# Kernel tuning notes

Hardware: AMD Instinct MI355X
Metric: run time of the kernel (lower is better)

The kernel has to match this reference:

```python
import jax, jax.numpy as jnp
import numpy as np

NUM_CLASSES = 16384
FEATURE_DIM = 128
LAMBDA_PARAM = 0.005
EPS = 1e-12  # matches torch F.normalize clamp_min eps


def setup_inputs() -> dict:
    key = jax.random.key(0)
    k1, k2 = jax.random.split(key)
    z = jax.random.normal(k1, (NUM_CLASSES, FEATURE_DIM), dtype=jnp.float32)
    labels = jax.random.randint(k2, (NUM_CLASSES,), 0, NUM_CLASSES, dtype=jnp.int32)
    return {"z": z, "labels": labels}


def _l2_normalize(x):
    # torch F.normalize(dim=1): x / max(||x||, eps); zero rows stay zero.
    n = jnp.linalg.norm(x, axis=1, keepdims=True)
    return x / jnp.maximum(n, EPS)


def reference(z, labels):
    # per-class mean via single segment reduce (replaces the per-class python loop)
    counts = jax.ops.segment_sum(jnp.ones_like(labels, dtype=z.dtype), labels,
                                 num_segments=NUM_CLASSES)            # [C]
    sums = jax.ops.segment_sum(z, labels, num_segments=NUM_CLASSES)   # [C, D]
    has = counts > 0
    centers = jnp.where(has[:, None], sums / jnp.maximum(counts, 1.0)[:, None], 0.0)

    z_norm = _l2_normalize(z)                 # [B, D]
    centers_norm = _l2_normalize(centers)     # [C, D]
    batch_size = z.shape[0]
    c = (z_norm @ centers_norm.T) / batch_size  # [B, C], square since B == C

    diag = jnp.diagonal(c)
    invariance_loss = jnp.sum((diag - 1.0) ** 2)
    redundancy_reduction_loss = jnp.sum(c ** 2) - jnp.sum(diag ** 2)  # off-diagonal sq sum
    return invariance_loss + LAMBDA_PARAM * redundancy_reduction_loss
```

## Files before the change

### kernel.cpp

```cpp
#include <hip/hip_runtime.h>
#include <hip/hip_fp16.h>

#define NC 16384
#define FD 128
#define LAMBDA 0.005f
#define SLOTCAP 64
#define NCH 256

typedef __attribute__((ext_vector_type(8))) short short8;
typedef __attribute__((ext_vector_type(4))) float f32x4;

__device__ __forceinline__ float wave_sum(float v) {
#pragma unroll
  for (int m = 32; m > 0; m >>= 1) v += __shfl_xor(v, m, 64);
  return v;
}

__global__ __launch_bounds__(256) void zero_kernel(int4* __restrict__ cnt4,
                                                   float* __restrict__ scal) {
  cnt4[blockIdx.x * 256 + threadIdx.x] = make_int4(0, 0, 0, 0);
  if (blockIdx.x == 0 && threadIdx.x < 16) scal[threadIdx.x] = 0.f;
}

__global__ __launch_bounds__(256) void scatter_kernel(
    const int* __restrict__ labels, int* __restrict__ cnt, int* __restrict__ slot) {
  int i = blockIdx.x * 256 + threadIdx.x;
  int lab = labels[i];
  int p = atomicAdd(&cnt[lab], 1);
  if (p < SLOTCAP) slot[(size_t)lab * SLOTCAP + p] = i;
}

__global__ __launch_bounds__(256) void center_kernel(
    const float* __restrict__ z, const int* __restrict__ cnt,
    const int* __restrict__ slot, float* __restrict__ cn,
    float2* __restrict__ dpart) {
  __shared__ float red[8];
  int t = threadIdx.x, wave = t >> 6, lane = t & 63;
  int c = blockIdx.x * 4 + wave;

  int n = cnt[c];
  if (n > SLOTCAP) n = SLOTCAP;
  float2 s = make_float2(0.f, 0.f);
  for (int k = 0; k < n; ++k) {
    int i = slot[(size_t)c * SLOTCAP + k];
    float2 v = *(const float2*)&z[(size_t)i * FD + lane * 2];
    s.x += v.x; s.y += v.y;
  }
  float inv = n > 0 ? 1.0f / (float)n : 0.0f;
  s.x *= inv; s.y *= inv;
  float sc = wave_sum(s.x * s.x + s.y * s.y);
  float ic = 1.0f / fmaxf(sqrtf(sc), 1e-12f);
  s.x *= ic; s.y *= ic;
  *(float2*)&cn[(size_t)c * FD + lane * 2] = s;

  float2 a = *(const float2*)&z[(size_t)c * FD + lane * 2];
  float na = wave_sum(a.x * a.x + a.y * a.y);
  float dd = wave_sum(a.x * s.x + a.y * s.y);
  float d = dd * (1.0f / fmaxf(sqrtf(na), 1e-12f));
  if (lane == 0) { red[wave * 2] = d; red[wave * 2 + 1] = d * d; }
  __syncthreads();
  if (t == 0) {
    dpart[blockIdx.x] = make_float2(red[0] + red[2] + red[4] + red[6],
                                    red[1] + red[3] + red[5] + red[7]);
  }
}

__global__ __launch_bounds__(256) void gram_kernel(
    const float* __restrict__ z, const float* __restrict__ cn,
    __half2* __restrict__ pz, __half2* __restrict__ pc) {
  __shared__ char lds[49920];
  unsigned short* B = (unsigned short*)lds;
  float* U = (float*)(lds + 16640);
  int t = threadIdx.x, wave = t >> 6, lane = t & 63;
  int b = blockIdx.x, m = b & 1, chunk = b >> 1;
  const float* A = m ? cn : z;

  {
    const float4* src = (const float4*)&A[(size_t)chunk * 64 * FD];
    float4* dst = (float4*)U;
#pragma unroll
    for (int k = 0; k < 8; ++k) dst[k * 256 + t] = src[k * 256 + t];
  }
  __syncthreads();
  {
    const float2* t2 = (const float2*)U;
#pragma unroll
    for (int j = 0; j < 16; ++j) {
      int row = wave * 16 + j;
      float2 v = t2[row * 64 + lane];
      float ss = wave_sum(v.x * v.x + v.y * v.y);
      float sc = 1.0f / fmaxf(sqrtf(ss), 1e-12f);
      v.x *= sc; v.y *= sc;
      unsigned ux = __float_as_uint(v.x), uy = __float_as_uint(v.y);
      ux = (ux + 0x7FFFu + ((ux >> 16) & 1u)) >> 16;
      uy = (uy + 0x7FFFu + ((uy >> 16) & 1u)) >> 16;
      *(unsigned*)&B[row * 130 + lane * 2] = ux | (uy << 16);
    }
  }
  __syncthreads();

  const unsigned short* Bl = B + (lane >> 4) * (8 * 130) + (lane & 15);
  short8 fr[2][8];
#pragma unroll
  for (int kb = 0; kb < 2; ++kb)
#pragma unroll
    for (int cb = 0; cb < 8; ++cb)
#pragma unroll
      for (int j = 0; j < 8; ++j)
        fr[kb][cb][j] = (short)Bl[kb * (32 * 130) + cb * 16 + j * 130];
  short8 fa[2][2];
#pragma unroll
  for (int til = 0; til < 2; ++til) {
    const unsigned short* Al = Bl + (wave * 2 + til) * 16;
#pragma unroll
    for (int kb = 0; kb < 2; ++kb)
#pragma unroll
      for (int j = 0; j < 8; ++j)
        fa[til][kb][j] = (short)Al[kb * (32 * 130) + j * 130];
  }

  f32x4 acc[2][8];
#pragma unroll
  for (int i = 0; i < 2; ++i)
#pragma unroll
    for (int j = 0; j < 8; ++j)
      acc[i][j] = (f32x4){0.f, 0.f, 0.f, 0.f};

#pragma unroll
  for (int til = 0; til < 2; ++til)
#pragma unroll
    for (int tj = 0; tj < 8; ++tj) {
      acc[til][tj] = __builtin_amdgcn_mfma_f32_16x16x32_bf16(
          fa[til][0], fr[0][tj], acc[til][tj], 0, 0, 0);
      acc[til][tj] = __builtin_amdgcn_mfma_f32_16x16x32_bf16(
          fa[til][1], fr[1][tj], acc[til][tj], 0, 0, 0);
    }

  unsigned short* G = (unsigned short*)(lds + 16640);
#pragma unroll
  for (int til = 0; til < 2; ++til)
#pragma unroll
    for (int tj = 0; tj < 8; ++tj)
#pragma unroll
      for (int q = 0; q < 4; ++q) {
        int d = (wave * 2 + til) * 16 + (lane >> 4) * 4 + q;
        int e = tj * 16 + (lane & 15);
        __half h = __float2half(acc[til][tj][q]);
        G[d * 130 + e] = *(unsigned short*)&h;
      }
  __syncthreads();

  unsigned* Pg = (unsigned*)((m ? pc : pz) + (size_t)chunk * 8192);
#pragma unroll
  for (int it = 0; it < 32; ++it) {
    int row = it * 4 + (t >> 6);
    int h2i = t & 63;
    Pg[row * 64 + h2i] = *(const unsigned*)(lds + 16640 + row * 260 + h2i * 4);
  }
}

__global__ __launch_bounds__(256) void reduce_final_kernel(
    const __half2* __restrict__ pz, const __half2* __restrict__ pc,
    const float2* __restrict__ dpart, float* __restrict__ scal,
    int* __restrict__ ticket_p, float* __restrict__ out) {
  __shared__ float2 lz[4][64], lc[4][64];
  __shared__ float rr[2][4];
  __shared__ int tk;
  int t = threadIdx.x, wave = t >> 6, lane = t & 63;
  int e2 = blockIdx.x * 64 + lane;
  float2 sz = make_float2(0.f, 0.f), sc = make_float2(0.f, 0.f);
  for (int k = 0; k < NCH / 4; ++k) {
    size_t c = (size_t)(wave * (NCH / 4) + k) * 8192 + e2;
    float2 fz = __half22float2(pz[c]);
    float2 fc = __half22float2(pc[c]);
    sz.x += fz.x; sz.y += fz.y;
    sc.x += fc.x; sc.y += fc.y;
  }
  lz[wave][lane] = sz;
  lc[wave][lane] = sc;
  __syncthreads();
  if (wave == 0) {
    float2 tz = make_float2(0.f, 0.f), tc = make_float2(0.f, 0.f);
#pragma unroll
    for (int w = 0; w < 4; ++w) {
      tz.x += lz[w][lane].x; tz.y += lz[w][lane].y;
      tc.x += lc[w][lane].x; tc.y += lc[w][lane].y;
    }
    float S = wave_sum(tz.x * tc.x + tz.y * tc.y);
    if (lane == 0) {
      unsafeAtomicAdd(&scal[2], S);
      __threadfence();
      tk = atomicAdd(ticket_p, 1);
    }
  }
  __syncthreads();
  if (tk == 127) {
    float a1 = 0.f, a2 = 0.f;
#pragma unroll
    for (int k = 0; k < 16; ++k) {
      float2 d = dpart[k * 256 + t];
      a1 += d.x; a2 += d.y;
    }
    a1 = wave_sum(a1);
    a2 = wave_sum(a2);
    if (lane == 0) { rr[0][wave] = a1; rr[1][wave] = a2; }
    __syncthreads();
    if (t == 0) {
      float SS = atomicAdd(&scal[2], 0.0f);
      double S1 = (double)rr[0][0] + rr[0][1] + rr[0][2] + rr[0][3];
      double S2 = (double)rr[1][0] + rr[1][1] + rr[1][2] + rr[1][3];
      double Sall = SS;
      double B = (double)NC;
      double inv_loss = S2 / (B * B) - 2.0 * S1 / B + (double)NC;
      double red_loss = (Sall - S2) / (B * B);
      out[0] = (float)(inv_loss + (double)LAMBDA * red_loss);
    }
  }
}

extern "C" void kernel_launch(void* const* d_in, const int* in_sizes, int n_in,
                              void* d_out, int out_size, void* d_ws, size_t ws_size,
                              hipStream_t stream) {
  const float* z = (const float*)d_in[0];
  const int* labels = (const int*)d_in[1];
  float* out = (float*)d_out;
  float* ws = (float*)d_ws;

  float* cn = ws;
  __half2* pz = (__half2*)(cn + (size_t)NC * FD);
  __half2* pc = pz + (size_t)NCH * 8192;
  float2* dpart = (float2*)(pc + (size_t)NCH * 8192);
  float* scal = (float*)(dpart + 4096);
  int* cnt = (int*)(scal + 16);
  int* slot = cnt + NC;
  int* ticket = (int*)&scal[8];

  zero_kernel<<<NC / 1024, 256, 0, stream>>>((int4*)cnt, scal);
  scatter_kernel<<<NC / 256, 256, 0, stream>>>(labels, cnt, slot);
  center_kernel<<<NC / 4, 256, 0, stream>>>(z, cnt, slot, cn, dpart);
  gram_kernel<<<2 * NCH, 256, 0, stream>>>(z, cn, pz, pc);
  reduce_final_kernel<<<128, 256, 0, stream>>>(pz, pc, dpart, scal, ticket, out);
}
```

Measured before the change: 46.64 us.

## Fuse normalization and bf16 packing into center kernel, halve gram partials

```diff
diff --git a/kernel.cpp b/kernel.cpp
--- a/kernel.cpp
+++ b/kernel.cpp
@@ -5,7 +5,7 @@
 #define FD 128
 #define LAMBDA 0.005f
 #define SLOTCAP 64
-#define NCH 256
+#define NPAIR 128
 
 typedef __attribute__((ext_vector_type(8))) short short8;
 typedef __attribute__((ext_vector_type(4))) float f32x4;
@@ -14,6 +14,13 @@
 #pragma unroll
   for (int m = 32; m > 0; m >>= 1) v += __shfl_xor(v, m, 64);
   return v;
+}
+
+__device__ __forceinline__ unsigned pack_bf16(float x, float y) {
+  unsigned ux = __float_as_uint(x), uy = __float_as_uint(y);
+  ux = (ux + 0x7FFFu + ((ux >> 16) & 1u)) >> 16;
+  uy = (uy + 0x7FFFu + ((uy >> 16) & 1u)) >> 16;
+  return ux | (uy << 16);
 }
 
 __global__ __launch_bounds__(256) void zero_kernel(int4* __restrict__ cnt4,
@@ -32,16 +39,29 @@
 
 __global__ __launch_bounds__(256) void center_kernel(
     const float* __restrict__ z, const int* __restrict__ cnt,
-    const int* __restrict__ slot, float* __restrict__ cn,
-    float2* __restrict__ dpart) {
+    const int* __restrict__ slot, unsigned* __restrict__ cnb,
+    unsigned* __restrict__ znb, float2* __restrict__ dpart) {
   __shared__ float red[8];
   int t = threadIdx.x, wave = t >> 6, lane = t & 63;
   int c = blockIdx.x * 4 + wave;
 
+  int4 s4 = *(const int4*)&slot[(size_t)c * SLOTCAP];
   int n = cnt[c];
+  float2 a = *(const float2*)&z[(size_t)c * FD + lane * 2];
   if (n > SLOTCAP) n = SLOTCAP;
+
+  int i0 = n > 0 ? s4.x : c, i1 = n > 1 ? s4.y : c;
+  int i2 = n > 2 ? s4.z : c, i3 = n > 3 ? s4.w : c;
+  float2 v0 = *(const float2*)&z[(size_t)i0 * FD + lane * 2];
+  float2 v1 = *(const float2*)&z[(size_t)i1 * FD + lane * 2];
+  float2 v2 = *(const float2*)&z[(size_t)i2 * FD + lane * 2];
+  float2 v3 = *(const float2*)&z[(size_t)i3 * FD + lane * 2];
   float2 s = make_float2(0.f, 0.f);
-  for (int k = 0; k < n; ++k) {
+  if (n > 0) { s.x += v0.x; s.y += v0.y; }
+  if (n > 1) { s.x += v1.x; s.y += v1.y; }
+  if (n > 2) { s.x += v2.x; s.y += v2.y; }
+  if (n > 3) { s.x += v3.x; s.y += v3.y; }
+  for (int k = 4; k < n; ++k) {
     int i = slot[(size_t)c * SLOTCAP + k];
     float2 v = *(const float2*)&z[(size_t)i * FD + lane * 2];
     s.x += v.x; s.y += v.y;
@@ -51,12 +71,14 @@
   float sc = wave_sum(s.x * s.x + s.y * s.y);
   float ic = 1.0f / fmaxf(sqrtf(sc), 1e-12f);
   s.x *= ic; s.y *= ic;
-  *(float2*)&cn[(size_t)c * FD + lane * 2] = s;
-
-  float2 a = *(const float2*)&z[(size_t)c * FD + lane * 2];
+  cnb[(size_t)c * 64 + lane] = pack_bf16(s.x, s.y);
+
   float na = wave_sum(a.x * a.x + a.y * a.y);
+  float ia = 1.0f / fmaxf(sqrtf(na), 1e-12f);
   float dd = wave_sum(a.x * s.x + a.y * s.y);
-  float d = dd * (1.0f / fmaxf(sqrtf(na), 1e-12f));
+  float d = dd * ia;
+  znb[(size_t)c * 64 + lane] = pack_bf16(a.x * ia, a.y * ia);
+
   if (lane == 0) { red[wave * 2] = d; red[wave * 2 + 1] = d * d; }
   __syncthreads();
   if (t == 0) {
@@ -66,58 +88,25 @@
 }
 
 __global__ __launch_bounds__(256) void gram_kernel(
-    const float* __restrict__ z, const float* __restrict__ cn,
+    const unsigned short* __restrict__ znb, const unsigned short* __restrict__ cnb,
     __half2* __restrict__ pz, __half2* __restrict__ pc) {
-  __shared__ char lds[49920];
-  unsigned short* B = (unsigned short*)lds;
-  float* U = (float*)(lds + 16640);
+  __shared__ char lds[33280];
+  unsigned short* Bu = (unsigned short*)lds;
   int t = threadIdx.x, wave = t >> 6, lane = t & 63;
-  int b = blockIdx.x, m = b & 1, chunk = b >> 1;
-  const float* A = m ? cn : z;
+  int b = blockIdx.x, m = b & 1, pair = b >> 1;
+  const unsigned short* Ab = m ? cnb : znb;
 
   {
-    const float4* src = (const float4*)&A[(size_t)chunk * 64 * FD];
-    float4* dst = (float4*)U;
-#pragma unroll
-    for (int k = 0; k < 8; ++k) dst[k * 256 + t] = src[k * 256 + t];
-  }
-  __syncthreads();
-  {
-    const float2* t2 = (const float2*)U;
-#pragma unroll
-    for (int j = 0; j < 16; ++j) {
-      int row = wave * 16 + j;
-      float2 v = t2[row * 64 + lane];
-      float ss = wave_sum(v.x * v.x + v.y * v.y);
-      float sc = 1.0f / fmaxf(sqrtf(ss), 1e-12f);
-      v.x *= sc; v.y *= sc;
-      unsigned ux = __float_as_uint(v.x), uy = __float_as_uint(v.y);
-      ux = (ux + 0x7FFFu + ((ux >> 16) & 1u)) >> 16;
-      uy = (uy + 0x7FFFu + ((uy >> 16) & 1u)) >> 16;
-      *(unsigned*)&B[row * 130 + lane * 2] = ux | (uy << 16);
-    }
-  }
-  __syncthreads();
-
-  const unsigned short* Bl = B + (lane >> 4) * (8 * 130) + (lane & 15);
-  short8 fr[2][8];
-#pragma unroll
-  for (int kb = 0; kb < 2; ++kb)
-#pragma unroll
-    for (int cb = 0; cb < 8; ++cb)
-#pragma unroll
-      for (int j = 0; j < 8; ++j)
-        fr[kb][cb][j] = (short)Bl[kb * (32 * 130) + cb * 16 + j * 130];
-  short8 fa[2][2];
-#pragma unroll
-  for (int til = 0; til < 2; ++til) {
-    const unsigned short* Al = Bl + (wave * 2 + til) * 16;
-#pragma unroll
-    for (int kb = 0; kb < 2; ++kb)
-#pragma unroll
-      for (int j = 0; j < 8; ++j)
-        fa[til][kb][j] = (short)Al[kb * (32 * 130) + j * 130];
-  }
+    const int4* src = (const int4*)(Ab + (size_t)pair * 16384);
+#pragma unroll
+    for (int k = 0; k < 8; ++k) {
+      int idx = k * 256 + t;
+      int q = idx >> 10, idx2 = idx & 1023;
+      int row = idx2 >> 4, col8 = idx2 & 15;
+      *(int4*)&Bu[q * 8320 + row * 130 + col8 * 8] = src[idx];
+    }
+  }
+  __syncthreads();
 
   f32x4 acc[2][8];
 #pragma unroll
@@ -127,16 +116,37 @@
       acc[i][j] = (f32x4){0.f, 0.f, 0.f, 0.f};
 
 #pragma unroll
-  for (int til = 0; til < 2; ++til)
-#pragma unroll
-    for (int tj = 0; tj < 8; ++tj) {
-      acc[til][tj] = __builtin_amdgcn_mfma_f32_16x16x32_bf16(
-          fa[til][0], fr[0][tj], acc[til][tj], 0, 0, 0);
-      acc[til][tj] = __builtin_amdgcn_mfma_f32_16x16x32_bf16(
-          fa[til][1], fr[1][tj], acc[til][tj], 0, 0, 0);
-    }
-
-  unsigned short* G = (unsigned short*)(lds + 16640);
+  for (int q = 0; q < 2; ++q) {
+    const unsigned short* Bl = Bu + q * 8320 + (lane >> 4) * (8 * 130) + (lane & 15);
+    short8 fr[2][8];
+#pragma unroll
+    for (int kb = 0; kb < 2; ++kb)
+#pragma unroll
+      for (int cb = 0; cb < 8; ++cb)
+#pragma unroll
+        for (int j = 0; j < 8; ++j)
+          fr[kb][cb][j] = (short)Bl[kb * 4160 + cb * 16 + j * 130];
+    short8 fa[2][2];
+#pragma unroll
+    for (int til = 0; til < 2; ++til)
+#pragma unroll
+      for (int kb = 0; kb < 2; ++kb)
+#pragma unroll
+        for (int j = 0; j < 8; ++j)
+          fa[til][kb][j] = (short)Bl[kb * 4160 + (wave * 2 + til) * 16 + j * 130];
+#pragma unroll
+    for (int til = 0; til < 2; ++til)
+#pragma unroll
+      for (int tj = 0; tj < 8; ++tj) {
+        acc[til][tj] = __builtin_amdgcn_mfma_f32_16x16x32_bf16(
+            fa[til][0], fr[0][tj], acc[til][tj], 0, 0, 0);
+        acc[til][tj] = __builtin_amdgcn_mfma_f32_16x16x32_bf16(
+            fa[til][1], fr[1][tj], acc[til][tj], 0, 0, 0);
+      }
+  }
+  __syncthreads();
+
+  unsigned short* G = (unsigned short*)lds;
 #pragma unroll
   for (int til = 0; til < 2; ++til)
 #pragma unroll
@@ -150,12 +160,12 @@
       }
   __syncthreads();
 
-  unsigned* Pg = (unsigned*)((m ? pc : pz) + (size_t)chunk * 8192);
+  unsigned* Pg = (unsigned*)((m ? pc : pz) + (size_t)pair * 8192);
 #pragma unroll
   for (int it = 0; it < 32; ++it) {
     int row = it * 4 + (t >> 6);
     int h2i = t & 63;
-    Pg[row * 64 + h2i] = *(const unsigned*)(lds + 16640 + row * 260 + h2i * 4);
+    Pg[row * 64 + h2i] = *(const unsigned*)(lds + row * 260 + h2i * 4);
   }
 }
 
@@ -169,8 +179,8 @@
   int t = threadIdx.x, wave = t >> 6, lane = t & 63;
   int e2 = blockIdx.x * 64 + lane;
   float2 sz = make_float2(0.f, 0.f), sc = make_float2(0.f, 0.f);
-  for (int k = 0; k < NCH / 4; ++k) {
-    size_t c = (size_t)(wave * (NCH / 4) + k) * 8192 + e2;
+  for (int k = 0; k < NPAIR / 4; ++k) {
+    size_t c = (size_t)(wave * (NPAIR / 4) + k) * 8192 + e2;
     float2 fz = __half22float2(pz[c]);
     float2 fc = __half22float2(pc[c]);
     sz.x += fz.x; sz.y += fz.y;
@@ -226,10 +236,11 @@
   float* out = (float*)d_out;
   float* ws = (float*)d_ws;
 
-  float* cn = ws;
-  __half2* pz = (__half2*)(cn + (size_t)NC * FD);
-  __half2* pc = pz + (size_t)NCH * 8192;
-  float2* dpart = (float2*)(pc + (size_t)NCH * 8192);
+  __half2* pz = (__half2*)ws;
+  __half2* pc = pz + (size_t)NPAIR * 8192;
+  unsigned* znb = (unsigned*)(pc + (size_t)NPAIR * 8192);
+  unsigned* cnb = znb + (size_t)NC * 64;
+  float2* dpart = (float2*)(cnb + (size_t)NC * 64);
   float* scal = (float*)(dpart + 4096);
   int* cnt = (int*)(scal + 16);
   int* slot = cnt + NC;
@@ -237,7 +248,8 @@
 
   zero_kernel<<<NC / 1024, 256, 0, stream>>>((int4*)cnt, scal);
   scatter_kernel<<<NC / 256, 256, 0, stream>>>(labels, cnt, slot);
-  center_kernel<<<NC / 4, 256, 0, stream>>>(z, cnt, slot, cn, dpart);
-  gram_kernel<<<2 * NCH, 256, 0, stream>>>(z, cn, pz, pc);
+  center_kernel<<<NC / 4, 256, 0, stream>>>(z, cnt, slot, cnb, znb, dpart);
+  gram_kernel<<<2 * NPAIR, 256, 0, stream>>>((const unsigned short*)znb,
+                                             (const unsigned short*)cnb, pz, pc);
   reduce_final_kernel<<<128, 256, 0, stream>>>(pz, pc, dpart, scal, ticket, out);
 }
```

Result: faster. 37.67 us, median of 2 (-19.2%).
